# Kernel tuning notes

Hardware: AMD Instinct MI355X
Metric: run time of the kernel (lower is better)

The kernel has to match this reference:

```python
import jax, jax.numpy as jnp
import numpy as np

N, E, G, D, F_IN, E_IN, H_EDGE, L, STEPS = 16384, 65536, 128, 64, 64, 16, 64, 3, 3
EPS = 1e-5


def setup_inputs() -> dict:
    key = jax.random.key(0)
    ks = jax.random.split(key, 24)
    def rn(k, shape, s=1.0):
        return jax.random.normal(k, shape, dtype=jnp.float32) * s
    inp = {
        'x': rn(ks[0], (N, F_IN)),
        'edge_index': jax.random.randint(ks[1], (2, E), 0, N, dtype=jnp.int32),
        'edge_attr': rn(ks[2], (E, E_IN)),
        'batch': ((jnp.arange(N, dtype=jnp.int32) * G) // N).astype(jnp.int32),
        # lin0
        'lin0_w': rn(ks[3], (F_IN, D), 0.1), 'lin0_b': rn(ks[4], (D,), 0.01),
        # per-layer edge MLP (16 -> 64 -> 64*64), stacked over L layers
        'mlp_w1': rn(ks[5], (L, E_IN, H_EDGE), 0.1), 'mlp_b1': rn(ks[6], (L, H_EDGE), 0.01),
        'mlp_w2': rn(ks[7], (L, H_EDGE, D * D), 0.02), 'mlp_b2': rn(ks[8], (L, D * D), 0.01),
        # NNConv root weight + bias
        'root_w': rn(ks[9], (L, D, D), 0.1), 'conv_b': rn(ks[10], (L, D), 0.01),
        # GraphNorm params
        'gn_w': jnp.ones((L, D), jnp.float32), 'gn_b': jnp.zeros((L, D), jnp.float32),
        'gn_scale': jnp.ones((L, D), jnp.float32),
        # Set2Set LSTM (input 2D -> hidden D), torch gate order i,f,g,o
        's2s_wih': rn(ks[11], (4 * D, 2 * D), 0.08), 's2s_whh': rn(ks[12], (4 * D, D), 0.08),
        's2s_bih': rn(ks[13], (4 * D,), 0.01), 's2s_bhh': rn(ks[14], (4 * D,), 0.01),
        # head: Linear(2D, D) -> ReLU -> Linear(D, 1)
        'head_w1': rn(ks[15], (2 * D, D), 0.08), 'head_b1': rn(ks[16], (D,), 0.01),
        'head_w2': rn(ks[17], (D, 1), 0.08), 'head_b2': rn(ks[18], (1,), 0.01),
    }
    return inp


def _seg_mean(vals, ids, num, counts):
    s = jax.ops.segment_sum(vals, ids, num_segments=num)
    return s / counts


def _forward(x, edge_index, edge_attr, batch, lin0_w, lin0_b, mlp_w1, mlp_b1,
             mlp_w2, mlp_b2, root_w, conv_b, gn_w, gn_b, gn_scale,
             s2s_wih, s2s_whh, s2s_bih, s2s_bhh, head_w1, head_b1, head_w2, head_b2):
    src, dst = edge_index[0], edge_index[1]
    n_counts = jnp.maximum(jax.ops.segment_sum(jnp.ones((E,), x.dtype), dst, num_segments=N), 1.0)[:, None]
    g_counts = jnp.maximum(jax.ops.segment_sum(jnp.ones((N,), x.dtype), batch, num_segments=G), 1.0)[:, None]

    x = jax.nn.relu(x @ lin0_w + lin0_b)
    for l in range(L):
        res = x
        # edge-conditioned weights: [E, D, D]
        h = jax.nn.relu(edge_attr @ mlp_w1[l] + mlp_b1[l])
        W = (h @ mlp_w2[l] + mlp_b2[l]).reshape(E, D, D)
        # per-edge matmul of gathered source features, mean-scatter to target
        msg = jnp.einsum('ed,edo->eo', x[src], W)
        agg = jax.ops.segment_sum(msg, dst, num_segments=N) / n_counts
        xc = jax.nn.relu(agg + x @ root_w[l] + conv_b[l])
        # GraphNorm: per-graph mean/var with learnable mean scale
        mean = _seg_mean(xc, batch, G, g_counts)
        sub = xc - gn_scale[l] * mean[batch]
        var = _seg_mean(sub * sub, batch, G, g_counts)
        xn = gn_w[l] * sub * jax.lax.rsqrt(var[batch] + EPS) + gn_b[l]
        x = xn + res  # dropout is identity in eval

    # Set2Set readout
    q_star = jnp.zeros((G, 2 * D), x.dtype)
    hh = jnp.zeros((G, D), x.dtype)
    cc = jnp.zeros((G, D), x.dtype)
    for _ in range(STEPS):
        gates = q_star @ s2s_wih.T + hh @ s2s_whh.T + s2s_bih + s2s_bhh
        i_g = jax.nn.sigmoid(gates[:, :D])
        f_g = jax.nn.sigmoid(gates[:, D:2 * D])
        g_g = jnp.tanh(gates[:, 2 * D:3 * D])
        o_g = jax.nn.sigmoid(gates[:, 3 * D:])
        cc = f_g * cc + i_g * g_g
        hh = o_g * jnp.tanh(cc)
        q = hh  # [G, D]
        e = jnp.sum(x * q[batch], axis=-1)  # [N]
        e_max = jax.ops.segment_max(e, batch, num_segments=G)
        ex = jnp.exp(e - e_max[batch])
        denom = jax.ops.segment_sum(ex, batch, num_segments=G)
        a = ex / denom[batch]
        r = jax.ops.segment_sum(a[:, None] * x, batch, num_segments=G)  # [G, D]
        q_star = jnp.concatenate([q, r], axis=-1)

    out = jax.nn.relu(q_star @ head_w1 + head_b1) @ head_w2 + head_b2
    return out.reshape(-1)


def reference(x, edge_index, edge_attr, batch, lin0_w, lin0_b, mlp_w1, mlp_b1,
              mlp_w2, mlp_b2, root_w, conv_b, gn_w, gn_b, gn_scale,
              s2s_wih, s2s_whh, s2s_bih, s2s_bhh, head_w1, head_b1, head_w2, head_b2):
    return _forward(x, edge_index, edge_attr, batch, lin0_w, lin0_b, mlp_w1, mlp_b1,
                    mlp_w2, mlp_b2, root_w, conv_b, gn_w, gn_b, gn_scale,
                    s2s_wih, s2s_whh, s2s_bih, s2s_bhh, head_w1, head_b1, head_w2, head_b2)
```

## Files before the change

### kernel.cpp

```cpp
#include <hip/hip_runtime.h>
#include <hip/hip_bf16.h>
#include <math.h>

#define N_NODES 16384
#define N_EDGES 65536
#define N_GRAPH 128
#define TNF 32
#define KC 4
#define NCH 16
#define CAP 160
#define MREG 10
#define E4 (N_EDGES * 4)
#define LFRAG 278528

typedef short s8v __attribute__((ext_vector_type(8)));
typedef float f4v __attribute__((ext_vector_type(4)));

__device__ __forceinline__ void splitw3(float v, unsigned short* h,
                                        unsigned short* m, unsigned short* l) {
    __hip_bfloat16 a = __float2bfloat16(v);
    float r1 = v - __bfloat162float(a);
    __hip_bfloat16 b = __float2bfloat16(r1);
    float r2 = r1 - __bfloat162float(b);
    __hip_bfloat16 c = __float2bfloat16(r2);
    *h = *reinterpret_cast<unsigned short*>(&a);
    *m = *reinterpret_cast<unsigned short*>(&b);
    *l = *reinterpret_cast<unsigned short*>(&c);
}

__global__ __launch_bounds__(256) void k_hist(const int* __restrict__ esrc,
                                              const int* __restrict__ edst,
                                              int* __restrict__ deg,
                                              int* __restrict__ cntd) {
    int i = blockIdx.x * 256 + threadIdx.x;
    if (i < N_EDGES) {
        atomicAdd(&deg[esrc[i]], 1);
        atomicAdd(&cntd[edst[i]], 1);
    }
}

__global__ __launch_bounds__(256) void k_scan2(const int* __restrict__ deg,
                                               const int* __restrict__ cntd,
                                               int* __restrict__ soff,
                                               int* __restrict__ doff,
                                               int* __restrict__ cur1,
                                               int* __restrict__ cur2) {
    const int* in = blockIdx.x ? cntd : deg;
    int* offs = blockIdx.x ? doff : soff;
    int* cur = blockIdx.x ? cur2 : cur1;
    __shared__ int part[256];
    int tid = threadIdx.x;
    int base = tid * 64;
    int s = 0;
    for (int i = 0; i < 64; ++i) s += in[base + i];
    part[tid] = s;
    __syncthreads();
    for (int d = 1; d < 256; d <<= 1) {
        int add = (tid >= d) ? part[tid - d] : 0;
        __syncthreads();
        part[tid] += add;
        __syncthreads();
    }
    int run = (tid == 0) ? 0 : part[tid - 1];
    for (int i = 0; i < 64; ++i) {
        offs[base + i] = run;
        cur[base + i] = run;
        run += in[base + i];
    }
    if (tid == 255) offs[N_NODES] = run;
}

__global__ __launch_bounds__(256) void k_fill_src(const int* __restrict__ esrc,
                                                  int* __restrict__ cursor,
                                                  int* __restrict__ ebs) {
    int i = blockIdx.x * 256 + threadIdx.x;
    if (i < N_EDGES) {
        int p = atomicAdd(&cursor[esrc[i]], 1);
        ebs[p] = i;
    }
}

__global__ __launch_bounds__(256) void k_sortseg(const int* __restrict__ offs,
                                                 int* __restrict__ arr) {
    int n = blockIdx.x * 256 + threadIdx.x;
    if (n >= N_NODES) return;
    int a = offs[n], b = offs[n + 1];
    for (int i = a + 1; i < b; ++i) {
        int v = arr[i], j = i - 1;
        while (j >= a && arr[j] > v) { arr[j + 1] = arr[j]; --j; }
        arr[j + 1] = v;
    }
}

__global__ __launch_bounds__(256) void k_fill_dl(const int* __restrict__ ebs,
                                                 const int* __restrict__ edst,
                                                 int* __restrict__ cursor2,
                                                 int* __restrict__ dlist) {
    int pos = blockIdx.x * 256 + threadIdx.x;
    if (pos < N_EDGES) {
        int e = ebs[pos];
        int p2 = atomicAdd(&cursor2[edst[e]], 1);
        dlist[p2] = pos;
    }
}

__global__ __launch_bounds__(256) void k_w2prep(const float* __restrict__ w2,
                                                const float* __restrict__ b2,
                                                unsigned short* __restrict__ w2fh,
                                                unsigned short* __restrict__ w2fm,
                                                unsigned short* __restrict__ w2fl) {
    __shared__ float sb[4096];
    int bid = blockIdx.x;
    int l = bid / 68, k = bid % 68;
    int tid = threadIdx.x;
    const float* src = nullptr;
    if (k < 64) src = w2 + (size_t)(l * 64 + k) * 4096;
    else if (k == 64) src = b2 + (size_t)l * 4096;
    if (src) {
        for (int i = 0; i < 4; ++i)
            *(f4v*)&sb[tid * 16 + i * 4] = *(const f4v*)(src + tid * 16 + i * 4);
    } else {
        for (int i = 0; i < 16; ++i) sb[tid * 16 + i] = 0.f;
    }
    __syncthreads();
    for (int slot = tid; slot < 512; slot += 256) {
        int s = slot >> 8;
        int rem = slot & 255;
        int o16 = rem >> 6;
        int lane = rem & 63;
        int frag = (k * 2 + s) * 4 + o16;
        unsigned short hv[8], mv[8], lv[8];
#pragma unroll
        for (int j = 0; j < 8; ++j) {
            float v = sb[(s * 32 + (lane >> 4) * 8 + j) * 64 + o16 * 16 + (lane & 15)];
            splitw3(v, &hv[j], &mv[j], &lv[j]);
        }
        size_t off = (size_t)l * LFRAG + frag * 512 + lane * 8;
#pragma unroll
        for (int j = 0; j < 8; ++j) {
            w2fh[off + j] = hv[j];
            w2fm[off + j] = mv[j];
            w2fl[off + j] = lv[j];
        }
    }
}

__global__ __launch_bounds__(256) void k_lin0(const float* __restrict__ xin,
                                              const float* __restrict__ w,
                                              const float* __restrict__ b,
                                              float* __restrict__ xout,
                                              unsigned short* __restrict__ xh,
                                              unsigned short* __restrict__ xm,
                                              unsigned short* __restrict__ xl) {
    __shared__ float As[64][64];
    __shared__ float Ws[64][64];
    __shared__ float bs[64];
    int tid = threadIdx.x;
    int n0 = blockIdx.x * 64;
    for (int i = tid; i < 1024; i += 256) {
        *(f4v*)&As[0][i * 4] = *(const f4v*)(xin + n0 * 64 + i * 4);
        *(f4v*)&Ws[0][i * 4] = *(const f4v*)(w + i * 4);
    }
    if (tid < 64) bs[tid] = b[tid];
    __syncthreads();
    int o = tid & 63, rr = tid >> 6;
    float acc[16];
#pragma unroll
    for (int i = 0; i < 16; ++i) acc[i] = bs[o];
    for (int d = 0; d < 64; ++d) {
        float wv = Ws[d][o];
#pragma unroll
        for (int i = 0; i < 16; ++i) acc[i] += As[rr * 16 + i][d] * wv;
    }
    for (int i = 0; i < 16; ++i) {
        int idx = (n0 + rr * 16 + i) * 64 + o;
        float v = fmaxf(acc[i], 0.f);
        xout[idx] = v;
        splitw3(v, &xh[idx], &xm[idx], &xl[idx]);
    }
}

__global__ __launch_bounds__(256) void k_hgemm(const float* __restrict__ ea,
                                               const float* __restrict__ w1,
                                               const float* __restrict__ b1,
                                               const int* __restrict__ ebs,
                                               float* __restrict__ h_s) {
    __shared__ float w1s[1024];
    __shared__ float b1s[64];
    __shared__ int eids[64];
    __shared__ float eas[64][20];
    int tid = threadIdx.x;
    int pos0 = blockIdx.x * 64;
    *(f4v*)&w1s[tid * 4] = *(const f4v*)(w1 + tid * 4);
    if (tid < 64) {
        b1s[tid] = b1[tid];
        eids[tid] = ebs[pos0 + tid];
    }
    __syncthreads();
    {
        int e = tid >> 2, part = tid & 3;
        f4v v = *(const f4v*)(ea + (size_t)eids[e] * 16 + part * 4);
        *(f4v*)&eas[e][part * 4] = v;
    }
    __syncthreads();
    int edge = tid >> 2, o16 = tid & 3;
    float acc[16];
#pragma unroll
    for (int j = 0; j < 16; ++j) acc[j] = b1s[o16 * 16 + j];
    for (int k = 0; k < 16; ++k) {
        float a = eas[edge][k];
#pragma unroll
        for (int j = 0; j < 16; ++j) acc[j] += a * w1s[k * 64 + o16 * 16 + j];
    }
    int pos = pos0 + edge;
#pragma unroll
    for (int cc = 0; cc < 4; ++cc) {
        int c = o16 * 4 + cc;
        f4v v;
#pragma unroll
        for (int j = 0; j < 4; ++j) v[j] = fmaxf(acc[cc * 4 + j], 0.f);
        *(f4v*)(h_s + c * E4 + pos * 4) = v;
    }
}

__device__ __forceinline__ void loadBh(int k, int ho, int lane,
                                       const unsigned short* __restrict__ wh,
                                       const unsigned short* __restrict__ wm,
                                       const unsigned short* __restrict__ wl,
                                       s8v (&B)[3][2][2]) {
#pragma unroll
    for (int s = 0; s < 2; ++s)
#pragma unroll
        for (int oo = 0; oo < 2; ++oo) {
            int fo = ((k * 2 + s) * 4 + (ho * 2 + oo)) * 512 + lane * 8;
            B[0][s][oo] = *(const s8v*)(wh + fo);
            B[1][s][oo] = *(const s8v*)(wm + fo);
            B[2][s][oo] = *(const s8v*)(wl + fo);
        }
}

__global__ __launch_bounds__(256, 2) void k_fused(
    const unsigned short* __restrict__ xh, const unsigned short* __restrict__ xm,
    const unsigned short* __restrict__ xl,
    const unsigned short* __restrict__ w2fh, const unsigned short* __restrict__ w2fm,
    const unsigned short* __restrict__ w2fl,
    const float* __restrict__ h_s, const int* __restrict__ soff,
    const int* __restrict__ ebs, const int* __restrict__ esrc,
    float* __restrict__ msg) {
    __shared__ __align__(16) float P[KC][TNF][68];
    __shared__ __align__(16) float hC[CAP][4];
    __shared__ short elt[CAP];

    const int tid = threadIdx.x;
    const int n0 = blockIdx.x * TNF;
    const int w = tid >> 6;
    const int lane = tid & 63;
    const int l15 = tid & 15;
    const int q = lane >> 4;
    const int grp = tid >> 4;

    const int e0 = soff[n0];
    const int cnt_full = soff[n0 + TNF] - e0;
    const int cnt = min(cnt_full, CAP);

    for (int i = tid; i < cnt; i += 256) elt[i] = (short)(esrc[ebs[e0 + i]] - n0);
    if (tid < cnt)
        *(f4v*)&hC[tid][0] = *(const f4v*)(h_s + (e0 + tid) * 4);

    s8v A[3][2][2];
#pragma unroll
    for (int rt = 0; rt < 2; ++rt)
#pragma unroll
        for (int s = 0; s < 2; ++s) {
            int n = n0 + rt * 16 + l15;
            int d0 = s * 32 + q * 8;
            A[0][rt][s] = *(const s8v*)(xh + n * 64 + d0);
            A[1][rt][s] = *(const s8v*)(xm + n * 64 + d0);
            A[2][rt][s] = *(const s8v*)(xl + n * 64 + d0);
        }

    s8v B0[3][2][2], B1[3][2][2];
    loadBh(w, 0, lane, w2fh, w2fm, w2fl, B0);

    const int cpg = (cnt + 15) >> 4;
    const int ib = grp * cpg;
    const int ie = min(ib + cpg, cnt);
    f4v m[MREG];
#pragma unroll
    for (int il = 0; il < MREG; ++il) m[il] = (f4v)0.f;

    __syncthreads();

    auto mfma_half = [&](s8v(&B)[3][2][2], int ho) {
#pragma unroll
        for (int rt = 0; rt < 2; ++rt) {
            f4v acc[2];
            acc[0] = (f4v)0.f;
            acc[1] = (f4v)0.f;
#pragma unroll
            for (int s = 0; s < 2; ++s)
#pragma unroll
                for (int oo = 0; oo < 2; ++oo) {
                    acc[oo] = __builtin_amdgcn_mfma_f32_16x16x32_bf16(A[0][rt][s], B[0][s][oo], acc[oo], 0, 0, 0);
                    acc[oo] = __builtin_amdgcn_mfma_f32_16x16x32_bf16(A[0][rt][s], B[1][s][oo], acc[oo], 0, 0, 0);
                    acc[oo] = __builtin_amdgcn_mfma_f32_16x16x32_bf16(A[1][rt][s], B[0][s][oo], acc[oo], 0, 0, 0);
                    acc[oo] = __builtin_amdgcn_mfma_f32_16x16x32_bf16(A[1][rt][s], B[1][s][oo], acc[oo], 0, 0, 0);
                    acc[oo] = __builtin_amdgcn_mfma_f32_16x16x32_bf16(A[0][rt][s], B[2][s][oo], acc[oo], 0, 0, 0);
                    acc[oo] = __builtin_amdgcn_mfma_f32_16x16x32_bf16(A[2][rt][s], B[0][s][oo], acc[oo], 0, 0, 0);
                }
#pragma unroll
            for (int oo = 0; oo < 2; ++oo)
#pragma unroll
                for (int r = 0; r < 4; ++r)
                    P[w][rt * 16 + q * 4 + r][(ho * 2 + oo) * 16 + l15] = acc[oo][r];
        }
    };

    for (int c = 0; c <= NCH; ++c) {
        const int k = c * KC + w;
        loadBh(k, 1, lane, w2fh, w2fm, w2fl, B1);
        mfma_half(B0, 0);
        if (c < NCH) loadBh((c + 1) * KC + w, 0, lane, w2fh, w2fm, w2fl, B0);
        f4v hn = (f4v)0.f;
        const bool hok = (c + 1 < NCH) && (tid < cnt);
        if (hok) hn = *(const f4v*)(h_s + (c + 1) * E4 + (e0 + tid) * 4);
        mfma_half(B1, 1);
        __syncthreads();
        if (c < NCH) {
            int tp = -1;
            f4v p0 = (f4v)0.f, p1 = (f4v)0.f, p2 = (f4v)0.f, p3 = (f4v)0.f;
#pragma unroll
            for (int il = 0; il < MREG; ++il) {
                int i = ib + il;
                if (i < ie) {
                    int t = elt[i];
                    if (t != tp) {
                        p0 = *(const f4v*)&P[0][t][l15 * 4];
                        p1 = *(const f4v*)&P[1][t][l15 * 4];
                        p2 = *(const f4v*)&P[2][t][l15 * 4];
                        p3 = *(const f4v*)&P[3][t][l15 * 4];
                        tp = t;
                    }
                    f4v hv = *(const f4v*)&hC[i][0];
                    m[il] += p0 * hv[0] + p1 * hv[1] + p2 * hv[2] + p3 * hv[3];
                }
            }
            for (int i = CAP + grp; i < cnt_full; i += 16) {
                int pos = e0 + i;
                int t = esrc[ebs[pos]] - n0;
                f4v hv = *(const f4v*)(h_s + c * E4 + pos * 4);
                f4v part = *(const f4v*)&P[0][t][l15 * 4] * hv[0] +
                           *(const f4v*)&P[1][t][l15 * 4] * hv[1] +
                           *(const f4v*)&P[2][t][l15 * 4] * hv[2] +
                           *(const f4v*)&P[3][t][l15 * 4] * hv[3];
                float* mp = msg + pos * 64 + l15 * 4;
                if (c == 0) *(f4v*)mp = part;
                else *(f4v*)mp = *(const f4v*)mp + part;
            }
        } else {
#pragma unroll
            for (int il = 0; il < MREG; ++il) {
                int i = ib + il;
                if (i < ie) m[il] += *(const f4v*)&P[0][elt[i]][l15 * 4];
            }
            for (int i = CAP + grp; i < cnt_full; i += 16) {
                int pos = e0 + i;
                int t = esrc[ebs[pos]] - n0;
                float* mp = msg + pos * 64 + l15 * 4;
                *(f4v*)mp = *(const f4v*)mp + *(const f4v*)&P[0][t][l15 * 4];
            }
        }
        __syncthreads();
        if (hok) *(f4v*)&hC[tid][0] = hn;
    }

#pragma unroll
    for (int il = 0; il < MREG; ++il) {
        int i = ib + il;
        if (i < ie) *(f4v*)(msg + (e0 + i) * 64 + l15 * 4) = m[il];
    }
}

__global__ __launch_bounds__(256) void k_agg(const float* __restrict__ msg,
                                             const int* __restrict__ dlist,
                                             const int* __restrict__ doff,
                                             float* __restrict__ agg) {
    int idx = blockIdx.x * 256 + threadIdx.x;
    int n = idx >> 6, o = idx & 63;
    int pa = doff[n], pb = doff[n + 1];
    float s = 0.f;
    for (int p = pa; p < pb; ++p) s += msg[(size_t)dlist[p] * 64 + o];
    agg[idx] = s / fmaxf((float)(pb - pa), 1.f);
}

__global__ __launch_bounds__(256) void k_conv_gn(
    const float* __restrict__ agg, const float* __restrict__ rootw,
    const float* __restrict__ convb, const float* __restrict__ gnsc,
    const float* __restrict__ gnw, const float* __restrict__ gnb,
    float* __restrict__ xb, unsigned short* __restrict__ xh,
    unsigned short* __restrict__ xm, unsigned short* __restrict__ xl) {
    __shared__ float xs[128][64];
    __shared__ float Ws[64][64];
    __shared__ float xcs[128][64];
    __shared__ float r1[4][64], r2[4][64], mv[64], rs[64];
    int g = blockIdx.x, tid = threadIdx.x;
    int o = tid & 63, rr = tid >> 6;
    int base = g * 128 * 64;
    for (int i = tid; i < 2048; i += 256) {
        *(f4v*)&xs[0][i * 4] = *(const f4v*)(xb + base + i * 4);
        if (i < 1024) *(f4v*)&Ws[0][i * 4] = *(const f4v*)(rootw + i * 4);
    }
    __syncthreads();
    float cb = convb[o];
    float ls = 0.f, ls2 = 0.f;
    for (int r = rr; r < 128; r += 4) {
        float acc = cb + agg[base + r * 64 + o];
        for (int d = 0; d < 64; ++d) acc += xs[r][d] * Ws[d][o];
        acc = fmaxf(acc, 0.f);
        xcs[r][o] = acc;
        ls += acc;
        ls2 += acc * acc;
    }
    r1[rr][o] = ls;
    r2[rr][o] = ls2;
    __syncthreads();
    if (tid < 64) {
        float sum = r1[0][tid] + r1[1][tid] + r1[2][tid] + r1[3][tid];
        float sum2 = r2[0][tid] + r2[1][tid] + r2[2][tid] + r2[3][tid];
        float m = sum * (1.f / 128.f);
        float ex2 = sum2 * (1.f / 128.f);
        float sc = gnsc[tid];
        float var = ex2 - (2.f * sc - sc * sc) * m * m;
        mv[tid] = m;
        rs[tid] = rsqrtf(var + 1e-5f);
    }
    __syncthreads();
    float sc = gnsc[o], wv = gnw[o], bv = gnb[o], mo = mv[o], rv = rs[o];
    for (int r = rr; r < 128; r += 4) {
        int idx = base + r * 64 + o;
        float xn = wv * (xcs[r][o] - sc * mo) * rv + bv + xs[r][o];
        xb[idx] = xn;
        splitw3(xn, &xh[idx], &xm[idx], &xl[idx]);
    }
}

__global__ __launch_bounds__(256) void k_s2s(const float* __restrict__ x,
                                             const float* __restrict__ wih,
                                             const float* __restrict__ whh,
                                             const float* __restrict__ bih,
                                             const float* __restrict__ bhh,
                                             const float* __restrict__ hw1,
                                             const float* __restrict__ hb1,
                                             const float* __restrict__ hw2,
                                             const float* __restrict__ hb2,
                                             float* __restrict__ out) {
    int g = blockIdx.x, tid = threadIdx.x;
    __shared__ float xg[128][64];
    __shared__ float qs[128];
    __shared__ float hhS[64], ccS[64];
    __shared__ float gl[256];
    __shared__ float ev[128];
    __shared__ float S[4][64];
    __shared__ float red[2];
    for (int i = tid; i < 8192; i += 256)
        xg[i >> 6][i & 63] = x[(g * 128 + (i >> 6)) * 64 + (i & 63)];
    if (tid < 128) qs[tid] = 0.f;
    if (tid < 64) { hhS[tid] = 0.f; ccS[tid] = 0.f; }
    __syncthreads();

    for (int step = 0; step < 3; ++step) {
        float acc = bih[tid] + bhh[tid];
        const float* wr = wih + tid * 128;
        for (int i = 0; i < 128; ++i) acc += qs[i] * wr[i];
        const float* w2r = whh + tid * 64;
        for (int i = 0; i < 64; ++i) acc += hhS[i] * w2r[i];
        gl[tid] = acc;
        __syncthreads();
        if (tid < 64) {
            float ig = 1.f / (1.f + expf(-gl[tid]));
            float fg = 1.f / (1.f + expf(-gl[64 + tid]));
            float gg = tanhf(gl[128 + tid]);
            float og = 1.f / (1.f + expf(-gl[192 + tid]));
            float cnew = fg * ccS[tid] + ig * gg;
            ccS[tid] = cnew;
            hhS[tid] = og * tanhf(cnew);
        }
        __syncthreads();
        if (tid < 128) {
            float s = 0.f;
            for (int c = 0; c < 64; ++c) s += xg[tid][c] * hhS[c];
            ev[tid] = s;
        }
        __syncthreads();
        if (tid < 64) {
            float mx = fmaxf(ev[tid], ev[tid + 64]);
            for (int off = 32; off > 0; off >>= 1) mx = fmaxf(mx, __shfl_down(mx, off));
            if (tid == 0) red[0] = mx;
        }
        __syncthreads();
        float emax = red[0];
        if (tid < 128) ev[tid] = expf(ev[tid] - emax);
        __syncthreads();
        if (tid < 64) {
            float sm = ev[tid] + ev[tid + 64];
            for (int off = 32; off > 0; off >>= 1) sm += __shfl_down(sm, off);
            if (tid == 0) red[1] = sm;
        }
        __syncthreads();
        float denom = red[1];
        int c = tid & 63, rr = tid >> 6;
        float p = 0.f;
        for (int n = rr; n < 128; n += 4) p += ev[n] * xg[n][c];
        S[rr][c] = p;
        __syncthreads();
        if (tid < 64) {
            float r = (S[0][tid] + S[1][tid] + S[2][tid] + S[3][tid]) / denom;
            qs[tid] = hhS[tid];
            qs[64 + tid] = r;
        }
        __syncthreads();
    }

    if (tid < 64) {
        float acc = hb1[tid];
        for (int i = 0; i < 128; ++i) acc += qs[i] * hw1[i * 64 + tid];
        acc = fmaxf(acc, 0.f);
        float v = acc * hw2[tid];
        for (int off = 32; off > 0; off >>= 1) v += __shfl_down(v, off);
        if (tid == 0) out[g] = v + hb2[0];
    }
}

extern "C" void kernel_launch(void* const* d_in, const int* in_sizes, int n_in,
                              void* d_out, int out_size, void* d_ws, size_t ws_size,
                              hipStream_t stream) {
    (void)in_sizes; (void)n_in; (void)out_size; (void)ws_size;
    const float* x_in  = (const float*)d_in[0];
    const int*   eidx  = (const int*)d_in[1];
    const float* eattr = (const float*)d_in[2];
    const float* lin0w = (const float*)d_in[4];
    const float* lin0b = (const float*)d_in[5];
    const float* mw1   = (const float*)d_in[6];
    const float* mb1   = (const float*)d_in[7];
    const float* mw2   = (const float*)d_in[8];
    const float* mb2   = (const float*)d_in[9];
    const float* rootw = (const float*)d_in[10];
    const float* convb = (const float*)d_in[11];
    const float* gnw   = (const float*)d_in[12];
    const float* gnb   = (const float*)d_in[13];
    const float* gnsc  = (const float*)d_in[14];
    const float* wih   = (const float*)d_in[15];
    const float* whh   = (const float*)d_in[16];
    const float* bih   = (const float*)d_in[17];
    const float* bhh   = (const float*)d_in[18];
    const float* hw1   = (const float*)d_in[19];
    const float* hb1   = (const float*)d_in[20];
    const float* hw2   = (const float*)d_in[21];
    const float* hb2   = (const float*)d_in[22];
    float* out = (float*)d_out;

    const int* esrc = eidx;
    const int* edst = eidx + N_EDGES;

    float* xb  = (float*)d_ws;
    float* h_s = xb + 1048576;
    float* agg = h_s;
    float* msg = h_s + 4194304;
    unsigned short* xh   = (unsigned short*)(msg + 4194304);
    unsigned short* xm   = xh + 1048576;
    unsigned short* xl   = xm + 1048576;
    unsigned short* w2fh = xl + 1048576;
    unsigned short* w2fm = w2fh + 3 * LFRAG;
    unsigned short* w2fl = w2fm + 3 * LFRAG;
    int* deg     = (int*)(w2fl + 3 * LFRAG);
    int* cntd    = deg + N_NODES;
    int* soff    = cntd + N_NODES;
    int* doff    = soff + (N_NODES + 1);
    int* cursor  = doff + (N_NODES + 1);
    int* cursor2 = cursor + N_NODES;
    int* ebs     = cursor2 + N_NODES;
    int* dlist   = ebs + N_EDGES;

    hipMemsetAsync(deg, 0, sizeof(int) * 2 * N_NODES, stream);

    k_w2prep<<<3 * 68, 256, 0, stream>>>(mw2, mb2, w2fh, w2fm, w2fl);
    k_hist<<<N_EDGES / 256, 256, 0, stream>>>(esrc, edst, deg, cntd);
    k_scan2<<<2, 256, 0, stream>>>(deg, cntd, soff, doff, cursor, cursor2);
    k_fill_src<<<N_EDGES / 256, 256, 0, stream>>>(esrc, cursor, ebs);
    k_sortseg<<<N_NODES / 256, 256, 0, stream>>>(soff, ebs);
    k_fill_dl<<<N_EDGES / 256, 256, 0, stream>>>(ebs, edst, cursor2, dlist);
    k_sortseg<<<N_NODES / 256, 256, 0, stream>>>(doff, dlist);

    k_lin0<<<N_NODES / 64, 256, 0, stream>>>(x_in, lin0w, lin0b, xb, xh, xm, xl);

    for (int l = 0; l < 3; ++l) {
        k_hgemm<<<N_EDGES / 64, 256, 0, stream>>>(eattr, mw1 + l * 1024, mb1 + l * 64,
                                                  ebs, h_s);
        k_fused<<<N_NODES / TNF, 256, 0, stream>>>(
            xh, xm, xl,
            w2fh + (size_t)l * LFRAG, w2fm + (size_t)l * LFRAG, w2fl + (size_t)l * LFRAG,
            h_s, soff, ebs, esrc, msg);
        k_agg<<<N_NODES * 64 / 256, 256, 0, stream>>>(msg, dlist, doff, agg);
        k_conv_gn<<<N_GRAPH, 256, 0, stream>>>(agg, rootw + l * 4096,
                                               convb + l * 64, gnsc + l * 64,
                                               gnw + l * 64, gnb + l * 64, xb,
                                               xh, xm, xl);
    }

    k_s2s<<<N_GRAPH, 256, 0, stream>>>(xb, wih, whh, bih, bhh,
                                       hw1, hb1, hw2, hb2, out);
}
```

Measured before the change: 526.0 us.

## Split fused NNConv kernel across two output-column halves per node tile

Launches two blocks per node tile, each computing only half of the 64 output columns, so the per-block B fragments, the P scratch tile and the per-thread message registers are halved (MREG 10 to 5, 32 edge groups of 8 lanes). The loop is restructured to ping-pong B0/B1 buffers across chunks instead of loading both halves each step. This doubles the grid for more occupancy and parallelism and lowers register pressure, at the cost of recomputing the A-side loads, edge lists and h_s reads in both blocks.

```diff
diff --git a/kernel.cpp b/kernel.cpp
--- a/kernel.cpp
+++ b/kernel.cpp
@@ -9,7 +9,7 @@
 #define KC 4
 #define NCH 16
 #define CAP 160
-#define MREG 10
+#define MREG 5
 #define E4 (N_EDGES * 4)
 #define LFRAG 278528
 
@@ -223,16 +223,16 @@
     }
 }
 
-__device__ __forceinline__ void loadBh(int k, int ho, int lane,
-                                       const unsigned short* __restrict__ wh,
-                                       const unsigned short* __restrict__ wm,
-                                       const unsigned short* __restrict__ wl,
-                                       s8v (&B)[3][2][2]) {
+__device__ __forceinline__ void loadB(int k, int oh, int lane,
+                                      const unsigned short* __restrict__ wh,
+                                      const unsigned short* __restrict__ wm,
+                                      const unsigned short* __restrict__ wl,
+                                      s8v (&B)[3][2][2]) {
 #pragma unroll
     for (int s = 0; s < 2; ++s)
 #pragma unroll
         for (int oo = 0; oo < 2; ++oo) {
-            int fo = ((k * 2 + s) * 4 + (ho * 2 + oo)) * 512 + lane * 8;
+            int fo = ((k * 2 + s) * 4 + (oh * 2 + oo)) * 512 + lane * 8;
             B[0][s][oo] = *(const s8v*)(wh + fo);
             B[1][s][oo] = *(const s8v*)(wm + fo);
             B[2][s][oo] = *(const s8v*)(wl + fo);
@@ -247,17 +247,20 @@
     const float* __restrict__ h_s, const int* __restrict__ soff,
     const int* __restrict__ ebs, const int* __restrict__ esrc,
     float* __restrict__ msg) {
-    __shared__ __align__(16) float P[KC][TNF][68];
+    __shared__ __align__(16) float P[KC][TNF][36];
     __shared__ __align__(16) float hC[CAP][4];
     __shared__ short elt[CAP];
 
     const int tid = threadIdx.x;
-    const int n0 = blockIdx.x * TNF;
+    const int tile = blockIdx.x >> 1;
+    const int oh = blockIdx.x & 1;
+    const int n0 = tile * TNF;
     const int w = tid >> 6;
     const int lane = tid & 63;
-    const int l15 = tid & 15;
+    const int l15 = lane & 15;
     const int q = lane >> 4;
-    const int grp = tid >> 4;
+    const int grp = tid >> 3;
+    const int l8 = tid & 7;
 
     const int e0 = soff[n0];
     const int cnt_full = soff[n0 + TNF] - e0;
@@ -280,9 +283,9 @@
         }
 
     s8v B0[3][2][2], B1[3][2][2];
-    loadBh(w, 0, lane, w2fh, w2fm, w2fl, B0);
-
-    const int cpg = (cnt + 15) >> 4;
+    loadB(w, oh, lane, w2fh, w2fm, w2fl, B0);
+
+    const int cpg = (cnt + 31) >> 5;
     const int ib = grp * cpg;
     const int ie = min(ib + cpg, cnt);
     f4v m[MREG];
@@ -291,7 +294,7 @@
 
     __syncthreads();
 
-    auto mfma_half = [&](s8v(&B)[3][2][2], int ho) {
+    auto mfma_chunk = [&](s8v(&B)[3][2][2]) {
 #pragma unroll
         for (int rt = 0; rt < 2; ++rt) {
             f4v acc[2];
@@ -312,19 +315,16 @@
             for (int oo = 0; oo < 2; ++oo)
 #pragma unroll
                 for (int r = 0; r < 4; ++r)
-                    P[w][rt * 16 + q * 4 + r][(ho * 2 + oo) * 16 + l15] = acc[oo][r];
+                    P[w][rt * 16 + q * 4 + r][oo * 16 + l15] = acc[oo][r];
         }
     };
 
-    for (int c = 0; c <= NCH; ++c) {
-        const int k = c * KC + w;
-        loadBh(k, 1, lane, w2fh, w2fm, w2fl, B1);
-        mfma_half(B0, 0);
-        if (c < NCH) loadBh((c + 1) * KC + w, 0, lane, w2fh, w2fm, w2fl, B0);
+    auto step = [&](int c, s8v(&BC)[3][2][2], s8v(&BN)[3][2][2]) {
+        if (c < NCH) loadB((c + 1) * KC + w, oh, lane, w2fh, w2fm, w2fl, BN);
         f4v hn = (f4v)0.f;
         const bool hok = (c + 1 < NCH) && (tid < cnt);
         if (hok) hn = *(const f4v*)(h_s + (c + 1) * E4 + (e0 + tid) * 4);
-        mfma_half(B1, 1);
+        mfma_chunk(BC);
         __syncthreads();
         if (c < NCH) {
             int tp = -1;
@@ -335,25 +335,25 @@
                 if (i < ie) {
                     int t = elt[i];
                     if (t != tp) {
-                        p0 = *(const f4v*)&P[0][t][l15 * 4];
-                        p1 = *(const f4v*)&P[1][t][l15 * 4];
-                        p2 = *(const f4v*)&P[2][t][l15 * 4];
-                        p3 = *(const f4v*)&P[3][t][l15 * 4];
+                        p0 = *(const f4v*)&P[0][t][l8 * 4];
+                        p1 = *(const f4v*)&P[1][t][l8 * 4];
+                        p2 = *(const f4v*)&P[2][t][l8 * 4];
+                        p3 = *(const f4v*)&P[3][t][l8 * 4];
                         tp = t;
                     }
                     f4v hv = *(const f4v*)&hC[i][0];
                     m[il] += p0 * hv[0] + p1 * hv[1] + p2 * hv[2] + p3 * hv[3];
                 }
             }
-            for (int i = CAP + grp; i < cnt_full; i += 16) {
+            for (int i = CAP + grp; i < cnt_full; i += 32) {
                 int pos = e0 + i;
                 int t = esrc[ebs[pos]] - n0;
                 f4v hv = *(const f4v*)(h_s + c * E4 + pos * 4);
-                f4v part = *(const f4v*)&P[0][t][l15 * 4] * hv[0] +
-                           *(const f4v*)&P[1][t][l15 * 4] * hv[1] +
-                           *(const f4v*)&P[2][t][l15 * 4] * hv[2] +
-                           *(const f4v*)&P[3][t][l15 * 4] * hv[3];
-                float* mp = msg + pos * 64 + l15 * 4;
+                f4v part = *(const f4v*)&P[0][t][l8 * 4] * hv[0] +
+                           *(const f4v*)&P[1][t][l8 * 4] * hv[1] +
+                           *(const f4v*)&P[2][t][l8 * 4] * hv[2] +
+                           *(const f4v*)&P[3][t][l8 * 4] * hv[3];
+                float* mp = msg + pos * 64 + oh * 32 + l8 * 4;
                 if (c == 0) *(f4v*)mp = part;
                 else *(f4v*)mp = *(const f4v*)mp + part;
             }
@@ -361,23 +361,28 @@
 #pragma unroll
             for (int il = 0; il < MREG; ++il) {
                 int i = ib + il;
-                if (i < ie) m[il] += *(const f4v*)&P[0][elt[i]][l15 * 4];
+                if (i < ie) m[il] += *(const f4v*)&P[0][elt[i]][l8 * 4];
             }
-            for (int i = CAP + grp; i < cnt_full; i += 16) {
+            for (int i = CAP + grp; i < cnt_full; i += 32) {
                 int pos = e0 + i;
                 int t = esrc[ebs[pos]] - n0;
-                float* mp = msg + pos * 64 + l15 * 4;
-                *(f4v*)mp = *(const f4v*)mp + *(const f4v*)&P[0][t][l15 * 4];
+                float* mp = msg + pos * 64 + oh * 32 + l8 * 4;
+                *(f4v*)mp = *(const f4v*)mp + *(const f4v*)&P[0][t][l8 * 4];
             }
         }
         __syncthreads();
         if (hok) *(f4v*)&hC[tid][0] = hn;
+    };
+
+    for (int cc = 0; cc <= NCH; cc += 2) {
+        step(cc, B0, B1);
+        if (cc + 1 <= NCH) step(cc + 1, B1, B0);
     }
 
 #pragma unroll
     for (int il = 0; il < MREG; ++il) {
         int i = ib + il;
-        if (i < ie) *(f4v*)(msg + (e0 + i) * 64 + l15 * 4) = m[il];
+        if (i < ie) *(f4v*)(msg + (e0 + i) * 64 + oh * 32 + l8 * 4) = m[il];
     }
 }
 
@@ -596,7 +601,7 @@
     for (int l = 0; l < 3; ++l) {
         k_hgemm<<<N_EDGES / 64, 256, 0, stream>>>(eattr, mw1 + l * 1024, mb1 + l * 64,
                                                   ebs, h_s);
-        k_fused<<<N_NODES / TNF, 256, 0, stream>>>(
+        k_fused<<<(N_NODES / TNF) * 2, 256, 0, stream>>>(
             xh, xm, xl,
             w2fh + (size_t)l * LFRAG, w2fm + (size_t)l * LFRAG, w2fl + (size_t)l * LFRAG,
             h_s, soff, ebs, esrc, msg);
```

New measurement: 555.1 us. +5.5%, slower.
